# Performance work log

Hardware: AMD Instinct MI355X
Metric: run time of the kernel (lower is better)

Reference implementation:

```python
import jax, jax.numpy as jnp
import numpy as np

NEG_SLOPE = 0.2


def add_self_loops(edge_index, num_nodes):
    loop = jnp.arange(num_nodes, dtype=edge_index.dtype)
    return jnp.concatenate([edge_index, jnp.stack([loop, loop])], axis=1)


def gat_conv(x, edge_index, W, att_src, att_dst, bias, heads, out_ch, concat):
    # x: [N, F_in]; edge_index: [2, E]; W: [F_in, heads*out_ch]
    # att_src/att_dst: [heads, out_ch]; bias: [heads*out_ch] or [out_ch]
    N = x.shape[0]
    ei = add_self_loops(edge_index, N)
    src, dst = ei[0], ei[1]
    xw = (x @ W).reshape(N, heads, out_ch)          # [N, H, C]
    a_src = jnp.einsum('nhc,hc->nh', xw, att_src)    # [N, H]
    a_dst = jnp.einsum('nhc,hc->nh', xw, att_dst)    # [N, H]
    e = a_src[src] + a_dst[dst]                      # [E', H]
    e = jax.nn.leaky_relu(e, NEG_SLOPE)
    # segment softmax over edges grouped by destination node
    e_max = jax.ops.segment_max(e, dst, num_segments=N)  # [N, H]
    e_exp = jnp.exp(e - e_max[dst])
    denom = jax.ops.segment_sum(e_exp, dst, num_segments=N)  # [N, H]
    alpha = e_exp / denom[dst]                       # [E', H]
    msg = xw[src] * alpha[:, :, None]                # [E', H, C]
    out = jax.ops.segment_sum(msg, dst, num_segments=N)  # [N, H, C]
    if concat:
        out = out.reshape(N, heads * out_ch)
    else:
        out = out.mean(axis=1)
    return out + bias


def setup_inputs() -> dict:
    key = jax.random.key(0)
    ks = jax.random.split(key, 10)
    N, E = 100000, 1600000
    F_in, hid, heads, F_out = 128, 32, 4, 40
    s = 0.1
    x = jax.random.normal(ks[0], (N, F_in), dtype=jnp.float32)
    edge_index = jax.random.randint(ks[1], (2, E), 0, N, dtype=jnp.int64)
    W1 = jax.random.normal(ks[2], (F_in, heads * hid), dtype=jnp.float32) * s
    att_src1 = jax.random.normal(ks[3], (heads, hid), dtype=jnp.float32) * s
    att_dst1 = jax.random.normal(ks[4], (heads, hid), dtype=jnp.float32) * s
    b1 = jax.random.normal(ks[5], (heads * hid,), dtype=jnp.float32) * s
    W2 = jax.random.normal(ks[6], (heads * hid, F_out), dtype=jnp.float32) * s
    att_src2 = jax.random.normal(ks[7], (1, F_out), dtype=jnp.float32) * s
    att_dst2 = jax.random.normal(ks[8], (1, F_out), dtype=jnp.float32) * s
    b2 = jax.random.normal(ks[9], (F_out,), dtype=jnp.float32) * s
    return {"x": x, "edge_index": edge_index, "W1": W1, "att_src1": att_src1,
            "att_dst1": att_dst1, "b1": b1, "W2": W2, "att_src2": att_src2,
            "att_dst2": att_dst2, "b2": b2}


def reference(x, edge_index, W1, att_src1, att_dst1, b1, W2, att_src2, att_dst2, b2):
    h = gat_conv(x, edge_index, W1, att_src1, att_dst1, b1, heads=4, out_ch=32, concat=True)
    h = jax.nn.relu(h)
    out = gat_conv(h, edge_index, W2, att_src2, att_dst2, b2, heads=1, out_ch=40, concat=True)
    return out
```

## Files before the change

kernel.cpp:

```cpp
#include <hip/hip_runtime.h>
#include <hip/hip_bf16.h>

#define NEG_SLOPE 0.2f
#define LOG2E 1.4426950408889634f
#define HWREG_XCC_ID_FULL (((32 - 1) << 11) | (0 << 6) | 20)

typedef _Float16 f16;
typedef f16 f16x8 __attribute__((ext_vector_type(8)));
typedef float f32x4 __attribute__((ext_vector_type(4)));

__device__ __forceinline__ unsigned pack_h2(float a, float b) {
    union { f16 h[2]; unsigned u; } c;
    c.h[0] = (f16)a; c.h[1] = (f16)b;
    return c.u;
}

__global__ void k_init(const int* __restrict__ ei32, int npairs, int* __restrict__ flag,
                       const float* __restrict__ W1, const float* __restrict__ W2,
                       f16* __restrict__ W1t, f16* __restrict__ W2t,
                       uint4* __restrict__ deg_part4, int nzero) {
    const int b = blockIdx.x, t = threadIdx.x;
    if (b == 0) {
        __shared__ int found;
        if (t == 0) found = 0;
        __syncthreads();
        for (int i = t; i < npairs; i += 256) {
            if (ei32[2 * i + 1] != 0) found = 1;
        }
        __syncthreads();
        if (t == 0) *flag = found ? 0 : 1;
    } else if (b <= 88) {
        int o = (b - 1) * 256 + t;
        if (o < 128 * 128) {
            int n = o >> 7, k = o & 127;
            W1t[o] = (f16)W1[k * 128 + n];
        } else {
            int o2 = o - 128 * 128;
            if (o2 < 48 * 128) {
                int n = o2 >> 7, k = o2 & 127;
                W2t[o2] = (f16)(n < 40 ? W2[k * 40 + n] : 0.f);
            }
        }
    } else {
        int idx = (b - 89) * 256 + t;
        if (idx < nzero) deg_part4[idx] = (uint4){0, 0, 0, 0};
    }
}

__global__ void k_degree(const void* __restrict__ ei, const int* __restrict__ flag,
                         int* __restrict__ deg_part, unsigned* __restrict__ packed,
                         int N, int E) {
    const int base = (blockIdx.x * blockDim.x + threadIdx.x) * 4;
    if (base >= E) return;
    const int f64 = *flag;
    const int xcc = (int)(__builtin_amdgcn_s_getreg(HWREG_XCC_ID_FULL) & 7u);
    int dv[4];
    if (f64) {
        const long long* p = (const long long*)ei + E;
#pragma unroll
        for (int k = 0; k < 4; k++) dv[k] = (base + k < E) ? (int)p[base + k] : 0;
    } else {
        const int* p = (const int*)ei + E;
#pragma unroll
        for (int k = 0; k < 4; k++) dv[k] = (base + k < E) ? p[base + k] : 0;
    }
    unsigned pk[4];
#pragma unroll
    for (int k = 0; k < 4; k++) {
        int lr = (base + k < E) ? atomicAdd(&deg_part[xcc * N + dv[k]], 1) : 0;
        pk[k] = ((unsigned)dv[k] << 15) | ((unsigned)xcc << 12) | (unsigned)lr;
    }
#pragma unroll
    for (int k = 0; k < 4; k++)
        if (base + k < E) packed[base + k] = pk[k];
}

__global__ __launch_bounds__(1024) void k_scan_blk(int* __restrict__ deg_part,
                                                   int* __restrict__ offsets,
                                                   int* __restrict__ blksum, int N) {
    __shared__ int wsums[16];
    const int t = threadIdx.x;
    const int lane = t & 63;
    const int wid = t >> 6;
    int idx = blockIdx.x * 4096 + t * 4;
    int v0 = 0, v1 = 0, v2 = 0, v3 = 0;
    if (((N & 3) == 0) && (idx + 3 < N)) {
        uint4 u[8];
#pragma unroll
        for (int x = 0; x < 8; x++) u[x] = *(uint4*)&deg_part[x * N + idx];
        int p0 = 0, p1 = 0, p2 = 0, p3 = 0;
#pragma unroll
        for (int x = 0; x < 8; x++) {
            uint4 w = u[x];
            u[x] = (uint4){(unsigned)p0, (unsigned)p1, (unsigned)p2, (unsigned)p3};
            p0 += (int)w.x; p1 += (int)w.y; p2 += (int)w.z; p3 += (int)w.w;
        }
#pragma unroll
        for (int x = 0; x < 8; x++) *(uint4*)&deg_part[x * N + idx] = u[x];
        v0 = p0; v1 = p1; v2 = p2; v3 = p3;
    } else if (idx < N) {
        int vv[4] = {0, 0, 0, 0};
        for (int i = 0; i < 4; i++) {
            int d = idx + i;
            if (d >= N) break;
            int p = 0;
#pragma unroll
            for (int x = 0; x < 8; x++) {
                int t0 = deg_part[x * N + d];
                deg_part[x * N + d] = p;
                p += t0;
            }
            vv[i] = p;
        }
        v0 = vv[0]; v1 = vv[1]; v2 = vv[2]; v3 = vv[3];
    }
    int s1 = v0 + v1, s2 = s1 + v2, s3 = s2 + v3;
    int inc = s3;
#pragma unroll
    for (int off = 1; off < 64; off <<= 1) {
        int y = __shfl_up(inc, off);
        if (lane >= off) inc += y;
    }
    if (lane == 63) wsums[wid] = inc;
    __syncthreads();
    if (wid == 0) {
        int v = (lane < 16) ? wsums[lane] : 0;
        int wi = v;
#pragma unroll
        for (int off = 1; off < 16; off <<= 1) {
            int y = __shfl_up(wi, off);
            if (lane >= off) wi += y;
        }
        if (lane < 16) wsums[lane] = wi - v;
        if (lane == 15) blksum[blockIdx.x] = wi;
    }
    __syncthreads();
    int excl = wsums[wid] + (inc - s3);
    if (idx + 0 < N) offsets[idx + 1] = excl + v0;
    if (idx + 1 < N) offsets[idx + 2] = excl + s1;
    if (idx + 2 < N) offsets[idx + 3] = excl + s2;
    if (idx + 3 < N) offsets[idx + 4] = excl + s3;
}

__global__ void k_scan_top(const int* __restrict__ blksum, int* __restrict__ blkoff, int G) {
    int l = threadIdx.x;
    int v = (l < G) ? blksum[l] : 0;
    int inc = v;
#pragma unroll
    for (int off = 1; off < 64; off <<= 1) {
        int y = __shfl_up(inc, off);
        if (l >= off) inc += y;
    }
    if (l < G) blkoff[l] = inc - v;
}

__global__ void k_scan_add(int* __restrict__ offsets, const int* __restrict__ blkoff, int N) {
    int n = blockIdx.x * blockDim.x + threadIdx.x;
    if (n >= N) return;
    offsets[n + 1] += blkoff[n >> 12];
    if (n == 0) offsets[0] = 0;
}

__global__ void k_scatter(const void* __restrict__ ei, const int* __restrict__ flag,
                          const int* __restrict__ offsets, const int* __restrict__ deg_part,
                          const unsigned* __restrict__ packed, int* __restrict__ csr_src,
                          int N, int E) {
    const int base = (blockIdx.x * blockDim.x + threadIdx.x) * 4;
    if (base >= E) return;
    const int f64 = *flag;
    int sv[4];
    if (f64) {
        const long long* p = (const long long*)ei;
#pragma unroll
        for (int k = 0; k < 4; k++) sv[k] = (base + k < E) ? (int)p[base + k] : 0;
    } else {
        const int* p = (const int*)ei;
#pragma unroll
        for (int k = 0; k < 4; k++) sv[k] = (base + k < E) ? p[base + k] : 0;
    }
    unsigned pk[4];
#pragma unroll
    for (int k = 0; k < 4; k++) pk[k] = (base + k < E) ? packed[base + k] : 0;
#pragma unroll
    for (int k = 0; k < 4; k++) {
        if (base + k < E) {
            unsigned u = pk[k];
            int d = (int)(u >> 15);
            int xcc = (int)((u >> 12) & 7u);
            int lr = (int)(u & 0xFFFu);
            csr_src[offsets[d] + deg_part[xcc * N + d] + lr] = sv[k];
        }
    }
}

__global__ __launch_bounds__(256) void k_gemm1(const float* __restrict__ X,
                                               const f16* __restrict__ W1t,
                                               const float* __restrict__ as1,
                                               const float* __restrict__ ad1,
                                               f16* __restrict__ Af,
                                               float* __restrict__ aS1,
                                               float* __restrict__ aD1, int N) {
    __shared__ f16 sA[64 * 136];
    __shared__ f16 sB[128 * 136];
    const int t = threadIdx.x;
    const int row0 = blockIdx.x * 64;

    {
        int r = t >> 2, seg = t & 3;
        int row = row0 + r;
        if (row >= N) row = N - 1;
        const float4* xg = (const float4*)(X + (size_t)row * 128 + seg * 32);
        unsigned tmp[16];
#pragma unroll
        for (int j = 0; j < 8; j++) {
            float4 v = xg[j];
            tmp[2 * j]     = pack_h2(v.x, v.y);
            tmp[2 * j + 1] = pack_h2(v.z, v.w);
        }
        uint4* dst = (uint4*)&sA[r * 136 + seg * 32];
#pragma unroll
        for (int j = 0; j < 4; j++) dst[j] = ((uint4*)tmp)[j];
        int n = t >> 1, half = (t & 1) * 64;
        const uint4* src = (const uint4*)(W1t + n * 128 + half);
        uint4* dw = (uint4*)&sB[n * 136 + half];
#pragma unroll
        for (int j = 0; j < 8; j++) dw[j] = src[j];
    }
    __syncthreads();

    const int w = t >> 6, lane = t & 63, ln = lane & 15, q = lane >> 4;
    f32x4 acc[8];
#pragma unroll
    for (int c = 0; c < 8; c++) acc[c] = (f32x4){0.f, 0.f, 0.f, 0.f};

#pragma unroll
    for (int ks = 0; ks < 4; ks++) {
        f16x8 a = *(const f16x8*)&sA[(w * 16 + ln) * 136 + ks * 32 + q * 8];
#pragma unroll
        for (int c = 0; c < 8; c++) {
            f16x8 b = *(const f16x8*)&sB[(c * 16 + ln) * 136 + ks * 32 + q * 8];
            acc[c] = __builtin_amdgcn_mfma_f32_16x16x32_f16(a, b, acc[c], 0, 0, 0);
        }
    }

#pragma unroll
    for (int c = 0; c < 8; c++)
#pragma unroll
        for (int reg = 0; reg < 4; reg++) {
            int rg = row0 + w * 16 + q * 4 + reg;
            if (rg < N) Af[(size_t)rg * 128 + c * 16 + ln] = (f16)acc[c][reg];
        }

    float ps[4][4], pd[4][4];
#pragma unroll
    for (int h = 0; h < 4; h++) {
        float as_lo = as1[32 * h + ln], as_hi = as1[32 * h + 16 + ln];
        float ad_lo = ad1[32 * h + ln], ad_hi = ad1[32 * h + 16 + ln];
#pragma unroll
        for (int reg = 0; reg < 4; reg++) {
            ps[h][reg] = acc[2 * h][reg] * as_lo + acc[2 * h + 1][reg] * as_hi;
            pd[h][reg] = acc[2 * h][reg] * ad_lo + acc[2 * h + 1][reg] * ad_hi;
        }
    }
#pragma unroll
    for (int h = 0; h < 4; h++)
#pragma unroll
        for (int reg = 0; reg < 4; reg++)
#pragma unroll
            for (int off = 1; off < 16; off <<= 1) {
                ps[h][reg] += __shfl_xor(ps[h][reg], off);
                pd[h][reg] += __shfl_xor(pd[h][reg], off);
            }
#pragma unroll
    for (int h = 0; h < 4; h++) {
        if (ln == 2 * h) {
#pragma unroll
            for (int reg = 0; reg < 4; reg++) {
                int rg = row0 + w * 16 + q * 4 + reg;
                if (rg < N) aS1[rg * 4 + h] = ps[h][reg] * LOG2E;
            }
        }
        if (ln == 2 * h + 1) {
#pragma unroll
            for (int reg = 0; reg < 4; reg++) {
                int rg = row0 + w * 16 + q * 4 + reg;
                if (rg < N) aD1[rg * 4 + h] = pd[h][reg] * LOG2E;
            }
        }
    }
}

__global__ __launch_bounds__(256) void k_gemm2(const f16* __restrict__ Hf,
                                               const f16* __restrict__ W2t,
                                               const float* __restrict__ as2,
                                               const float* __restrict__ ad2,
                                               f16* __restrict__ X2f,
                                               float* __restrict__ aS2,
                                               float* __restrict__ aD2, int N) {
    __shared__ f16 sA[64 * 136];
    __shared__ f16 sB[48 * 136];
    const int t = threadIdx.x;
    const int row0 = blockIdx.x * 64;
    {
        int r = t >> 2, seg = t & 3;
        int row = row0 + r;
        if (row >= N) row = N - 1;
        const uint4* hg = (const uint4*)(Hf + (size_t)row * 128 + seg * 32);
        uint4* dst = (uint4*)&sA[r * 136 + seg * 32];
#pragma unroll
        for (int j = 0; j < 4; j++) dst[j] = hg[j];
        const uint4* wsrc = (const uint4*)W2t;
#pragma unroll
        for (int u = t; u < 768; u += 256) {
            int o = u * 8;
            int n = o >> 7, ko = o & 127;
            *(uint4*)&sB[n * 136 + ko] = wsrc[u];
        }
    }
    __syncthreads();

    const int w = t >> 6, lane = t & 63, ln = lane & 15, q = lane >> 4;
    f32x4 acc[3];
#pragma unroll
    for (int c = 0; c < 3; c++) acc[c] = (f32x4){0.f, 0.f, 0.f, 0.f};

#pragma unroll
    for (int ks = 0; ks < 4; ks++) {
        f16x8 a = *(const f16x8*)&sA[(w * 16 + ln) * 136 + ks * 32 + q * 8];
#pragma unroll
        for (int c = 0; c < 3; c++) {
            f16x8 b = *(const f16x8*)&sB[(c * 16 + ln) * 136 + ks * 32 + q * 8];
            acc[c] = __builtin_amdgcn_mfma_f32_16x16x32_f16(a, b, acc[c], 0, 0, 0);
        }
    }

#pragma unroll
    for (int c = 0; c < 3; c++) {
        int col = c * 16 + ln;
        if (col < 40) {
#pragma unroll
            for (int reg = 0; reg < 4; reg++) {
                int rg = row0 + w * 16 + q * 4 + reg;
                if (rg < N) X2f[(size_t)rg * 64 + col] = (f16)acc[c][reg];
            }
        } else {
#pragma unroll
            for (int reg = 0; reg < 4; reg++) {
                int rg = row0 + w * 16 + q * 4 + reg;
                if (rg < N) X2f[(size_t)rg * 64 + col] = (f16)0.f;
            }
        }
    }
    {
        int col = 48 + ln;
#pragma unroll
        for (int reg = 0; reg < 4; reg++) {
            int rg = row0 + w * 16 + q * 4 + reg;
            if (rg < N) X2f[(size_t)rg * 64 + col] = (f16)0.f;
        }
    }

    float ps[4], pd[4];
#pragma unroll
    for (int reg = 0; reg < 4; reg++) { ps[reg] = 0.f; pd[reg] = 0.f; }
#pragma unroll
    for (int c = 0; c < 3; c++) {
        int col = c * 16 + ln;
        float as_ = (col < 40) ? as2[col] : 0.f;
        float ad_ = (col < 40) ? ad2[col] : 0.f;
#pragma unroll
        for (int reg = 0; reg < 4; reg++) {
            ps[reg] = fmaf(acc[c][reg], as_, ps[reg]);
            pd[reg] = fmaf(acc[c][reg], ad_, pd[reg]);
        }
    }
#pragma unroll
    for (int reg = 0; reg < 4; reg++) {
#pragma unroll
        for (int off = 1; off < 16; off <<= 1) {
            ps[reg] += __shfl_xor(ps[reg], off);
            pd[reg] += __shfl_xor(pd[reg], off);
        }
        int rg = row0 + w * 16 + q * 4 + reg;
        if (rg < N) {
            if (ln == 0) aS2[rg] = ps[reg] * LOG2E;
            if (ln == 1) aD2[rg] = pd[reg] * LOG2E;
        }
    }
}

__global__ __launch_bounds__(256) void k_msg1(const int* __restrict__ offsets,
                                              const int* __restrict__ csr_src,
                                              const float* __restrict__ aS,
                                              const float* __restrict__ aD,
                                              const f16* __restrict__ Af,
                                              const float* __restrict__ b1,
                                              f16* __restrict__ Hf, int N) {
    const int lane = threadIdx.x & 63;
    const int n = blockIdx.x * 4 + (threadIdx.x >> 6);
    const bool node_ok = (n < N);
    const int g = lane >> 4;
    const int p = lane & 15;
    const int h = p >> 2;

    int b = 0, e = 0;
    float adh = 0.f;
    if (node_ok) {
        b = offsets[n];
        e = offsets[n + 1];
        adh = aD[n * 4 + h];
    }

    float acc[8];
#pragma unroll
    for (int k = 0; k < 8; k++) acc[k] = 0.f;
    float wsum = 0.f;

    if (node_ok) {
        float xs = aS[n * 4 + h] + adh;
        float ws = __builtin_amdgcn_exp2f(fmaxf(xs, NEG_SLOPE * xs));
        if (g != 0) ws = 0.f;
        const f16x8 hv = *(const f16x8*)(Af + (size_t)n * 128 + p * 8);
#pragma unroll
        for (int k = 0; k < 8; k++) acc[k] = fmaf(ws, (float)hv[k], acc[k]);
        wsum = ws;
    }

    int sreg = 0;
    if (node_ok && e > b) {
        int idx = b + lane;
        if (idx >= e) idx = e - 1;
        sreg = csr_src[idx];
    }

    int i = b;
#pragma unroll 2
    for (; i < e && (i - b) + 4 <= 64; i += 4) {
        int j = i + g;
        bool valid = (j < e);
        int s = __builtin_amdgcn_ds_bpermute((j - b) << 2, sreg);
        if (!valid) s = 0;
        float sv = aS[s * 4 + h];
        const f16x8 hv = *(const f16x8*)(Af + (size_t)s * 128 + p * 8);
        float x = sv + adh;
        float wgt = __builtin_amdgcn_exp2f(fmaxf(x, NEG_SLOPE * x));
        if (!valid) wgt = 0.f;
#pragma unroll
        for (int k = 0; k < 8; k++) acc[k] = fmaf(wgt, (float)hv[k], acc[k]);
        wsum += wgt;
    }
    for (; i < e; i += 4) {
        int j = i + g;
        bool valid = (j < e);
        int jc = valid ? j : (e - 1);
        int s = csr_src[jc];
        if (!valid) s = 0;
        float sv = aS[s * 4 + h];
        const f16x8 hv = *(const f16x8*)(Af + (size_t)s * 128 + p * 8);
        float x = sv + adh;
        float wgt = __builtin_amdgcn_exp2f(fmaxf(x, NEG_SLOPE * x));
        if (!valid) wgt = 0.f;
#pragma unroll
        for (int k = 0; k < 8; k++) acc[k] = fmaf(wgt, (float)hv[k], acc[k]);
        wsum += wgt;
    }

#pragma unroll
    for (int k = 0; k < 8; k++) {
        acc[k] += __shfl_xor(acc[k], 16);
        acc[k] += __shfl_xor(acc[k], 32);
    }
    wsum += __shfl_xor(wsum, 16);
    wsum += __shfl_xor(wsum, 32);

    if (node_ok && g == 0) {
        float inv = __builtin_amdgcn_rcpf(wsum);
        const float4* bb = (const float4*)(b1 + p * 8);
        float4 b0 = bb[0], b4 = bb[1];
        float bv[8] = {b0.x, b0.y, b0.z, b0.w, b4.x, b4.y, b4.z, b4.w};
        union { f16 h8[8]; uint4 u; } o;
#pragma unroll
        for (int k = 0; k < 8; k++) {
            float v = fmaf(acc[k], inv, bv[k]);
            o.h8[k] = (f16)fmaxf(v, 0.f);
        }
        *(uint4*)(Hf + (size_t)n * 128 + p * 8) = o.u;
    }
}

__global__ __launch_bounds__(256) void k_msg2(const int* __restrict__ offsets,
                                              const int* __restrict__ csr_src,
                                              const float* __restrict__ aS,
                                              const float* __restrict__ aD,
                                              const f16* __restrict__ X2f,
                                              const float* __restrict__ b2,
                                              float* __restrict__ OUT, int N) {
    const int lane = threadIdx.x & 63;
    const int n = blockIdx.x * 4 + (threadIdx.x >> 6);
    const bool node_ok = (n < N);
    const int g = lane >> 3;
    const int p = lane & 7;

    int b = 0, e = 0;
    float adh = 0.f;
    if (node_ok) {
        b = offsets[n];
        e = offsets[n + 1];
        adh = aD[n];
    }

    float acc[8];
#pragma unroll
    for (int k = 0; k < 8; k++) acc[k] = 0.f;
    float wsum = 0.f;

    if (node_ok) {
        float xs = aS[n] + adh;
        float ws = __builtin_amdgcn_exp2f(fmaxf(xs, NEG_SLOPE * xs));
        if (g != 0) ws = 0.f;
        const f16x8 hv = *(const f16x8*)(X2f + (size_t)n * 64 + p * 8);
#pragma unroll
        for (int k = 0; k < 8; k++) acc[k] = fmaf(ws, (float)hv[k], acc[k]);
        wsum = ws;
    }

    int sreg = 0;
    if (node_ok && e > b) {
        int idx = b + lane;
        if (idx >= e) idx = e - 1;
        sreg = csr_src[idx];
    }

    int i = b;
#pragma unroll 2
    for (; i < e && (i - b) + 8 <= 64; i += 8) {
        int j = i + g;
        bool valid = (j < e);
        int s = __builtin_amdgcn_ds_bpermute((j - b) << 2, sreg);
        if (!valid) s = 0;
        float sv = aS[s];
        const f16x8 hv = *(const f16x8*)(X2f + (size_t)s * 64 + p * 8);
        float x = sv + adh;
        float wgt = __builtin_amdgcn_exp2f(fmaxf(x, NEG_SLOPE * x));
        if (!valid) wgt = 0.f;
#pragma unroll
        for (int k = 0; k < 8; k++) acc[k] = fmaf(wgt, (float)hv[k], acc[k]);
        wsum += wgt;
    }
    for (; i < e; i += 8) {
        int j = i + g;
        bool valid = (j < e);
        int jc = valid ? j : (e - 1);
        int s = csr_src[jc];
        if (!valid) s = 0;
        float sv = aS[s];
        const f16x8 hv = *(const f16x8*)(X2f + (size_t)s * 64 + p * 8);
        float x = sv + adh;
        float wgt = __builtin_amdgcn_exp2f(fmaxf(x, NEG_SLOPE * x));
        if (!valid) wgt = 0.f;
#pragma unroll
        for (int k = 0; k < 8; k++) acc[k] = fmaf(wgt, (float)hv[k], acc[k]);
        wsum += wgt;
    }

#pragma unroll
    for (int k = 0; k < 8; k++) {
        acc[k] += __shfl_xor(acc[k], 8);
        acc[k] += __shfl_xor(acc[k], 16);
        acc[k] += __shfl_xor(acc[k], 32);
    }
    wsum += __shfl_xor(wsum, 8);
    wsum += __shfl_xor(wsum, 16);
    wsum += __shfl_xor(wsum, 32);

    if (node_ok && g == 0 && p < 5) {
        float inv = __builtin_amdgcn_rcpf(wsum);
        const float4* bb = (const float4*)(b2 + p * 8);
        float4 b0 = bb[0], b4 = bb[1];
        float bv[8] = {b0.x, b0.y, b0.z, b0.w, b4.x, b4.y, b4.z, b4.w};
        float4 o0, o1;
        o0.x = fmaf(acc[0], inv, bv[0]); o0.y = fmaf(acc[1], inv, bv[1]);
        o0.z = fmaf(acc[2], inv, bv[2]); o0.w = fmaf(acc[3], inv, bv[3]);
        o1.x = fmaf(acc[4], inv, bv[4]); o1.y = fmaf(acc[5], inv, bv[5]);
        o1.z = fmaf(acc[6], inv, bv[6]); o1.w = fmaf(acc[7], inv, bv[7]);
        float* op = OUT + (size_t)n * 40 + p * 8;
        *(float4*)op = o0;
        *(float4*)(op + 4) = o1;
    }
}

extern "C" void kernel_launch(void* const* d_in, const int* in_sizes, int n_in,
                              void* d_out, int out_size, void* d_ws, size_t ws_size,
                              hipStream_t stream) {
    const float* x   = (const float*)d_in[0];
    const void*  ei  = d_in[1];
    const float* W1  = (const float*)d_in[2];
    const float* as1 = (const float*)d_in[3];
    const float* ad1 = (const float*)d_in[4];
    const float* b1  = (const float*)d_in[5];
    const float* W2  = (const float*)d_in[6];
    const float* as2 = (const float*)d_in[7];
    const float* ad2 = (const float*)d_in[8];
    const float* b2  = (const float*)d_in[9];
    float* out = (float*)d_out;

    const int N = in_sizes[0] / 128;
    const int E = in_sizes[1] / 2;

    char* w = (char*)d_ws;
    auto alloc = [&](size_t bytes) {
        char* p = w;
        w += (bytes + 15) & ~(size_t)15;
        return p;
    };
    int* flag        = (int*)alloc(16);
    int* offsets     = (int*)alloc((size_t)(N + 1) * 4);
    int* deg_part    = (int*)alloc((size_t)N * 8 * 4);
    unsigned* packed = (unsigned*)alloc((size_t)E * 4);
    int* csr_src     = (int*)alloc((size_t)E * 4);
    int* blksum      = (int*)alloc(64 * 4);
    int* blkoff      = (int*)alloc(64 * 4);
    float* aS1       = (float*)alloc((size_t)N * 4 * 4);
    float* aD1       = (float*)alloc((size_t)N * 4 * 4);
    float* aS2       = (float*)alloc((size_t)N * 4);
    float* aD2       = (float*)alloc((size_t)N * 4);
    f16* W1t         = (f16*)alloc(128 * 128 * 2);
    f16* W2t         = (f16*)alloc(48 * 128 * 2);
    f16* Af          = (f16*)alloc((size_t)N * 128 * 2);
    f16* X2f         = (f16*)alloc((size_t)N * 64 * 2);
    f16* Hf          = (f16*)alloc((size_t)N * 128 * 2);

    const int nzero = 2 * N;
    k_init<<<89 + (nzero + 255) / 256, 256, 0, stream>>>(
        (const int*)ei, 1024, flag, W1, W2, W1t, W2t, (uint4*)deg_part, nzero);

    k_degree<<<(E + 1023) / 1024, 256, 0, stream>>>(ei, flag, deg_part, packed, N, E);
    const int G = (N + 4095) / 4096;
    k_scan_blk<<<G, 1024, 0, stream>>>(deg_part, offsets, blksum, N);
    k_scan_top<<<1, 64, 0, stream>>>(blksum, blkoff, G);
    k_scan_add<<<(N + 255) / 256, 256, 0, stream>>>(offsets, blkoff, N);
    k_scatter<<<(E + 1023) / 1024, 256, 0, stream>>>(ei, flag, offsets, deg_part,
                                                     packed, csr_src, N, E);

    const int gb = (N + 63) / 64;
    k_gemm1<<<gb, 256, 0, stream>>>(x, W1t, as1, ad1, Af, aS1, aD1, N);
    k_msg1<<<(N + 3) / 4, 256, 0, stream>>>(offsets, csr_src, aS1, aD1, Af, b1, Hf, N);

    k_gemm2<<<gb, 256, 0, stream>>>(Hf, W2t, as2, ad2, X2f, aS2, aD2, N);
    k_msg2<<<(N + 3) / 4, 256, 0, stream>>>(offsets, csr_src, aS2, aD2, X2f, b2, out, N);
}
```

Baseline: 395.2 us.

## Fuse CSR construction kernels into one cooperative grid-synced kernel

Result: slower. 977.6 us (+147.4%).

```diff
diff --git a/kernel.cpp b/kernel.cpp
--- a/kernel.cpp
+++ b/kernel.cpp
@@ -1,9 +1,14 @@
 #include <hip/hip_runtime.h>
 #include <hip/hip_bf16.h>
+#include <hip/hip_cooperative_groups.h>
+
+namespace cg = cooperative_groups;
 
 #define NEG_SLOPE 0.2f
 #define LOG2E 1.4426950408889634f
 #define HWREG_XCC_ID_FULL (((32 - 1) << 11) | (0 << 6) | 20)
+
+#define CSR_GRID 1024
 
 typedef _Float16 f16;
 typedef f16 f16x8 __attribute__((ext_vector_type(8)));
@@ -15,74 +20,77 @@
     return c.u;
 }
 
-__global__ void k_init(const int* __restrict__ ei32, int npairs, int* __restrict__ flag,
-                       const float* __restrict__ W1, const float* __restrict__ W2,
-                       f16* __restrict__ W1t, f16* __restrict__ W2t,
-                       uint4* __restrict__ deg_part4, int nzero) {
-    const int b = blockIdx.x, t = threadIdx.x;
-    if (b == 0) {
-        __shared__ int found;
+__global__ __launch_bounds__(256) void k_csr(const int* __restrict__ ei32,
+                                             const void* __restrict__ ei,
+                                             int* __restrict__ flag,
+                                             const float* __restrict__ W1,
+                                             const float* __restrict__ W2,
+                                             f16* __restrict__ W1t,
+                                             f16* __restrict__ W2t,
+                                             int* __restrict__ deg_part,
+                                             unsigned* __restrict__ packed,
+                                             int* __restrict__ offsets,
+                                             int* __restrict__ blksum,
+                                             int* __restrict__ blkoff,
+                                             int* __restrict__ csr_src,
+                                             int N, int E) {
+    cg::grid_group grid = cg::this_grid();
+    __shared__ int wsums[4];
+    __shared__ int found;
+    const int B = blockIdx.x, t = threadIdx.x;
+    const int gsize = gridDim.x * blockDim.x;
+    const int gid = B * blockDim.x + t;
+    const int lane = t & 63, wid = t >> 6;
+
+    if (B == 0) {
         if (t == 0) found = 0;
         __syncthreads();
-        for (int i = t; i < npairs; i += 256) {
+        for (int i = t; i < 1024; i += 256)
             if (ei32[2 * i + 1] != 0) found = 1;
-        }
         __syncthreads();
         if (t == 0) *flag = found ? 0 : 1;
-    } else if (b <= 88) {
-        int o = (b - 1) * 256 + t;
+    }
+    for (int o = gid; o < 128 * 128 + 48 * 128; o += gsize) {
         if (o < 128 * 128) {
             int n = o >> 7, k = o & 127;
             W1t[o] = (f16)W1[k * 128 + n];
         } else {
             int o2 = o - 128 * 128;
-            if (o2 < 48 * 128) {
-                int n = o2 >> 7, k = o2 & 127;
-                W2t[o2] = (f16)(n < 40 ? W2[k * 40 + n] : 0.f);
-            }
-        }
-    } else {
-        int idx = (b - 89) * 256 + t;
-        if (idx < nzero) deg_part4[idx] = (uint4){0, 0, 0, 0};
-    }
-}
-
-__global__ void k_degree(const void* __restrict__ ei, const int* __restrict__ flag,
-                         int* __restrict__ deg_part, unsigned* __restrict__ packed,
-                         int N, int E) {
-    const int base = (blockIdx.x * blockDim.x + threadIdx.x) * 4;
-    if (base >= E) return;
+            int n = o2 >> 7, k = o2 & 127;
+            W2t[o2] = (f16)(n < 40 ? W2[k * 40 + n] : 0.f);
+        }
+    }
+    {
+        uint4* dp4 = (uint4*)deg_part;
+        for (int i = gid; i < 2 * N; i += gsize) dp4[i] = (uint4){0, 0, 0, 0};
+    }
+    grid.sync();
+
     const int f64 = *flag;
     const int xcc = (int)(__builtin_amdgcn_s_getreg(HWREG_XCC_ID_FULL) & 7u);
-    int dv[4];
-    if (f64) {
-        const long long* p = (const long long*)ei + E;
-#pragma unroll
-        for (int k = 0; k < 4; k++) dv[k] = (base + k < E) ? (int)p[base + k] : 0;
-    } else {
-        const int* p = (const int*)ei + E;
-#pragma unroll
-        for (int k = 0; k < 4; k++) dv[k] = (base + k < E) ? p[base + k] : 0;
-    }
-    unsigned pk[4];
-#pragma unroll
-    for (int k = 0; k < 4; k++) {
-        int lr = (base + k < E) ? atomicAdd(&deg_part[xcc * N + dv[k]], 1) : 0;
-        pk[k] = ((unsigned)dv[k] << 15) | ((unsigned)xcc << 12) | (unsigned)lr;
-    }
-#pragma unroll
-    for (int k = 0; k < 4; k++)
-        if (base + k < E) packed[base + k] = pk[k];
-}
-
-__global__ __launch_bounds__(1024) void k_scan_blk(int* __restrict__ deg_part,
-                                                   int* __restrict__ offsets,
-                                                   int* __restrict__ blksum, int N) {
-    __shared__ int wsums[16];
-    const int t = threadIdx.x;
-    const int lane = t & 63;
-    const int wid = t >> 6;
-    int idx = blockIdx.x * 4096 + t * 4;
+    for (int base = gid * 4; base < E; base += gsize * 4) {
+        int dv[4];
+        if (f64) {
+            const long long* p = (const long long*)ei + E;
+#pragma unroll
+            for (int k = 0; k < 4; k++) dv[k] = (base + k < E) ? (int)p[base + k] : 0;
+        } else {
+            const int* p = (const int*)ei + E;
+#pragma unroll
+            for (int k = 0; k < 4; k++) dv[k] = (base + k < E) ? p[base + k] : 0;
+        }
+#pragma unroll
+        for (int k = 0; k < 4; k++) {
+            if (base + k < E) {
+                int lr = atomicAdd(&deg_part[xcc * N + dv[k]], 1);
+                packed[base + k] = ((unsigned)dv[k] << 15) | ((unsigned)xcc << 12) |
+                                   (unsigned)lr;
+            }
+        }
+    }
+    grid.sync();
+
+    const int idx = gid * 4;
     int v0 = 0, v1 = 0, v2 = 0, v3 = 0;
     if (((N & 3) == 0) && (idx + 3 < N)) {
         uint4 u[8];
@@ -114,7 +122,7 @@
         }
         v0 = vv[0]; v1 = vv[1]; v2 = vv[2]; v3 = vv[3];
     }
-    int s1 = v0 + v1, s2 = s1 + v2, s3 = s2 + v3;
+    const int s1 = v0 + v1, s2 = s1 + v2, s3 = s2 + v3;
     int inc = s3;
 #pragma unroll
     for (int off = 1; off < 64; off <<= 1) {
@@ -124,71 +132,81 @@
     if (lane == 63) wsums[wid] = inc;
     __syncthreads();
     if (wid == 0) {
-        int v = (lane < 16) ? wsums[lane] : 0;
+        int v = (lane < 4) ? wsums[lane] : 0;
         int wi = v;
 #pragma unroll
-        for (int off = 1; off < 16; off <<= 1) {
+        for (int off = 1; off < 4; off <<= 1) {
             int y = __shfl_up(wi, off);
             if (lane >= off) wi += y;
         }
-        if (lane < 16) wsums[lane] = wi - v;
-        if (lane == 15) blksum[blockIdx.x] = wi;
+        if (lane < 4) wsums[lane] = wi - v;
+        if (lane == 3) blksum[B] = wi;
     }
     __syncthreads();
-    int excl = wsums[wid] + (inc - s3);
-    if (idx + 0 < N) offsets[idx + 1] = excl + v0;
-    if (idx + 1 < N) offsets[idx + 2] = excl + s1;
-    if (idx + 2 < N) offsets[idx + 3] = excl + s2;
-    if (idx + 3 < N) offsets[idx + 4] = excl + s3;
-}
-
-__global__ void k_scan_top(const int* __restrict__ blksum, int* __restrict__ blkoff, int G) {
-    int l = threadIdx.x;
-    int v = (l < G) ? blksum[l] : 0;
-    int inc = v;
-#pragma unroll
-    for (int off = 1; off < 64; off <<= 1) {
-        int y = __shfl_up(inc, off);
-        if (l >= off) inc += y;
-    }
-    if (l < G) blkoff[l] = inc - v;
-}
-
-__global__ void k_scan_add(int* __restrict__ offsets, const int* __restrict__ blkoff, int N) {
-    int n = blockIdx.x * blockDim.x + threadIdx.x;
-    if (n >= N) return;
-    offsets[n + 1] += blkoff[n >> 12];
-    if (n == 0) offsets[0] = 0;
-}
-
-__global__ void k_scatter(const void* __restrict__ ei, const int* __restrict__ flag,
-                          const int* __restrict__ offsets, const int* __restrict__ deg_part,
-                          const unsigned* __restrict__ packed, int* __restrict__ csr_src,
-                          int N, int E) {
-    const int base = (blockIdx.x * blockDim.x + threadIdx.x) * 4;
-    if (base >= E) return;
-    const int f64 = *flag;
-    int sv[4];
-    if (f64) {
-        const long long* p = (const long long*)ei;
-#pragma unroll
-        for (int k = 0; k < 4; k++) sv[k] = (base + k < E) ? (int)p[base + k] : 0;
-    } else {
-        const int* p = (const int*)ei;
-#pragma unroll
-        for (int k = 0; k < 4; k++) sv[k] = (base + k < E) ? p[base + k] : 0;
-    }
-    unsigned pk[4];
-#pragma unroll
-    for (int k = 0; k < 4; k++) pk[k] = (base + k < E) ? packed[base + k] : 0;
-#pragma unroll
-    for (int k = 0; k < 4; k++) {
-        if (base + k < E) {
-            unsigned u = pk[k];
-            int d = (int)(u >> 15);
-            int xcc = (int)((u >> 12) & 7u);
-            int lr = (int)(u & 0xFFFu);
-            csr_src[offsets[d] + deg_part[xcc * N + d] + lr] = sv[k];
+    const int excl_local = wsums[wid] + (inc - s3);
+    grid.sync();
+
+    if (B == 0) {
+        int i = t * 4;
+        int b0 = blksum[i], b1 = blksum[i + 1], b2 = blksum[i + 2], b3 = blksum[i + 3];
+        int t1 = b0 + b1, t2 = t1 + b2, t3 = t2 + b3;
+        int inc2 = t3;
+#pragma unroll
+        for (int off = 1; off < 64; off <<= 1) {
+            int y = __shfl_up(inc2, off);
+            if (lane >= off) inc2 += y;
+        }
+        if (lane == 63) wsums[wid] = inc2;
+        __syncthreads();
+        if (wid == 0) {
+            int v = (lane < 4) ? wsums[lane] : 0;
+            int wi = v;
+#pragma unroll
+            for (int off = 1; off < 4; off <<= 1) {
+                int y = __shfl_up(wi, off);
+                if (lane >= off) wi += y;
+            }
+            if (lane < 4) wsums[lane] = wi - v;
+        }
+        __syncthreads();
+        int ex2 = wsums[wid] + (inc2 - t3);
+        blkoff[i] = ex2;
+        blkoff[i + 1] = ex2 + b0;
+        blkoff[i + 2] = ex2 + t1;
+        blkoff[i + 3] = ex2 + t2;
+    }
+    grid.sync();
+
+    {
+        const int boff = blkoff[B] + excl_local;
+        if (idx + 0 < N) offsets[idx + 1] = boff + v0;
+        if (idx + 1 < N) offsets[idx + 2] = boff + s1;
+        if (idx + 2 < N) offsets[idx + 3] = boff + s2;
+        if (idx + 3 < N) offsets[idx + 4] = boff + s3;
+        if (gid == 0) offsets[0] = 0;
+    }
+    grid.sync();
+
+    for (int base = gid * 4; base < E; base += gsize * 4) {
+        int sv[4];
+        if (f64) {
+            const long long* p = (const long long*)ei;
+#pragma unroll
+            for (int k = 0; k < 4; k++) sv[k] = (base + k < E) ? (int)p[base + k] : 0;
+        } else {
+            const int* p = (const int*)ei;
+#pragma unroll
+            for (int k = 0; k < 4; k++) sv[k] = (base + k < E) ? p[base + k] : 0;
+        }
+#pragma unroll
+        for (int k = 0; k < 4; k++) {
+            if (base + k < E) {
+                unsigned u = packed[base + k];
+                int d = (int)(u >> 15);
+                int xc = (int)((u >> 12) & 7u);
+                int lr = (int)(u & 0xFFFu);
+                csr_src[offsets[d] + deg_part[xc * N + d] + lr] = sv[k];
+            }
         }
     }
 }
@@ -618,8 +636,8 @@
     int* deg_part    = (int*)alloc((size_t)N * 8 * 4);
     unsigned* packed = (unsigned*)alloc((size_t)E * 4);
     int* csr_src     = (int*)alloc((size_t)E * 4);
-    int* blksum      = (int*)alloc(64 * 4);
-    int* blkoff      = (int*)alloc(64 * 4);
+    int* blksum      = (int*)alloc((size_t)CSR_GRID * 4);
+    int* blkoff      = (int*)alloc((size_t)CSR_GRID * 4);
     float* aS1       = (float*)alloc((size_t)N * 4 * 4);
     float* aD1       = (float*)alloc((size_t)N * 4 * 4);
     float* aS2       = (float*)alloc((size_t)N * 4);
@@ -630,17 +648,18 @@
     f16* X2f         = (f16*)alloc((size_t)N * 64 * 2);
     f16* Hf          = (f16*)alloc((size_t)N * 128 * 2);
 
-    const int nzero = 2 * N;
-    k_init<<<89 + (nzero + 255) / 256, 256, 0, stream>>>(
-        (const int*)ei, 1024, flag, W1, W2, W1t, W2t, (uint4*)deg_part, nzero);
-
-    k_degree<<<(E + 1023) / 1024, 256, 0, stream>>>(ei, flag, deg_part, packed, N, E);
-    const int G = (N + 4095) / 4096;
-    k_scan_blk<<<G, 1024, 0, stream>>>(deg_part, offsets, blksum, N);
-    k_scan_top<<<1, 64, 0, stream>>>(blksum, blkoff, G);
-    k_scan_add<<<(N + 255) / 256, 256, 0, stream>>>(offsets, blkoff, N);
-    k_scatter<<<(E + 1023) / 1024, 256, 0, stream>>>(ei, flag, offsets, deg_part,
-                                                     packed, csr_src, N, E);
+    {
+        const int* ei32 = (const int*)ei;
+        const void* eiv = ei;
+        int Nv = N, Ev = E;
+        void* args[] = {(void*)&ei32, (void*)&eiv, (void*)&flag,
+                        (void*)&W1, (void*)&W2, (void*)&W1t, (void*)&W2t,
+                        (void*)&deg_part, (void*)&packed, (void*)&offsets,
+                        (void*)&blksum, (void*)&blkoff, (void*)&csr_src,
+                        (void*)&Nv, (void*)&Ev};
+        hipLaunchCooperativeKernel((void*)k_csr, dim3(CSR_GRID), dim3(256),
+                                   args, 0, stream);
+    }
 
     const int gb = (N + 63) / 64;
     k_gemm1<<<gb, 256, 0, stream>>>(x, W1t, as1, ad1, Af, aS1, aD1, N);
```

## Fuse three-kernel prefix scan into single-pass decoupled scan

Applied to the files above, without the earlier changes.

Result: no change. 393.7 us (-0.4%).

```diff
diff --git a/kernel.cpp b/kernel.cpp
--- a/kernel.cpp
+++ b/kernel.cpp
@@ -18,11 +18,13 @@
 __global__ void k_init(const int* __restrict__ ei32, int npairs, int* __restrict__ flag,
                        const float* __restrict__ W1, const float* __restrict__ W2,
                        f16* __restrict__ W1t, f16* __restrict__ W2t,
-                       uint4* __restrict__ deg_part4, int nzero) {
+                       uint4* __restrict__ deg_part4, int nzero,
+                       int* __restrict__ partials) {
     const int b = blockIdx.x, t = threadIdx.x;
     if (b == 0) {
         __shared__ int found;
         if (t == 0) found = 0;
+        if (t < 64) partials[t] = 0;
         __syncthreads();
         for (int i = t; i < npairs; i += 256) {
             if (ei32[2 * i + 1] != 0) found = 1;
@@ -75,14 +77,16 @@
         if (base + k < E) packed[base + k] = pk[k];
 }
 
-__global__ __launch_bounds__(1024) void k_scan_blk(int* __restrict__ deg_part,
-                                                   int* __restrict__ offsets,
-                                                   int* __restrict__ blksum, int N) {
+__global__ __launch_bounds__(1024) void k_scan(int* __restrict__ deg_part,
+                                               int* __restrict__ offsets,
+                                               int* __restrict__ partials, int N) {
     __shared__ int wsums[16];
+    __shared__ int bprefix;
     const int t = threadIdx.x;
     const int lane = t & 63;
     const int wid = t >> 6;
-    int idx = blockIdx.x * 4096 + t * 4;
+    const int B = blockIdx.x;
+    int idx = B * 4096 + t * 4;
     int v0 = 0, v1 = 0, v2 = 0, v3 = 0;
     if (((N & 3) == 0) && (idx + 3 < N)) {
         uint4 u[8];
@@ -114,7 +118,7 @@
         }
         v0 = vv[0]; v1 = vv[1]; v2 = vv[2]; v3 = vv[3];
     }
-    int s1 = v0 + v1, s2 = s1 + v2, s3 = s2 + v3;
+    const int s1 = v0 + v1, s2 = s1 + v2, s3 = s2 + v3;
     int inc = s3;
 #pragma unroll
     for (int off = 1; off < 64; off <<= 1) {
@@ -132,33 +136,30 @@
             if (lane >= off) wi += y;
         }
         if (lane < 16) wsums[lane] = wi - v;
-        if (lane == 15) blksum[blockIdx.x] = wi;
+        int tot = __shfl(wi, 15);
+        if (lane == 0)
+            __hip_atomic_store(&partials[B], tot + 1, __ATOMIC_RELEASE,
+                               __HIP_MEMORY_SCOPE_AGENT);
+        int pre = 0;
+        for (int i = lane; i < B; i += 64) {
+            int vr;
+            do {
+                vr = __hip_atomic_load(&partials[i], __ATOMIC_ACQUIRE,
+                                       __HIP_MEMORY_SCOPE_AGENT);
+            } while (vr == 0);
+            pre += vr - 1;
+        }
+#pragma unroll
+        for (int off = 1; off < 64; off <<= 1) pre += __shfl_xor(pre, off);
+        if (lane == 0) bprefix = pre;
     }
     __syncthreads();
-    int excl = wsums[wid] + (inc - s3);
+    const int excl = bprefix + wsums[wid] + (inc - s3);
     if (idx + 0 < N) offsets[idx + 1] = excl + v0;
     if (idx + 1 < N) offsets[idx + 2] = excl + s1;
     if (idx + 2 < N) offsets[idx + 3] = excl + s2;
     if (idx + 3 < N) offsets[idx + 4] = excl + s3;
-}
-
-__global__ void k_scan_top(const int* __restrict__ blksum, int* __restrict__ blkoff, int G) {
-    int l = threadIdx.x;
-    int v = (l < G) ? blksum[l] : 0;
-    int inc = v;
-#pragma unroll
-    for (int off = 1; off < 64; off <<= 1) {
-        int y = __shfl_up(inc, off);
-        if (l >= off) inc += y;
-    }
-    if (l < G) blkoff[l] = inc - v;
-}
-
-__global__ void k_scan_add(int* __restrict__ offsets, const int* __restrict__ blkoff, int N) {
-    int n = blockIdx.x * blockDim.x + threadIdx.x;
-    if (n >= N) return;
-    offsets[n + 1] += blkoff[n >> 12];
-    if (n == 0) offsets[0] = 0;
+    if (B == 0 && t == 0) offsets[0] = 0;
 }
 
 __global__ void k_scatter(const void* __restrict__ ei, const int* __restrict__ flag,
@@ -618,8 +619,7 @@
     int* deg_part    = (int*)alloc((size_t)N * 8 * 4);
     unsigned* packed = (unsigned*)alloc((size_t)E * 4);
     int* csr_src     = (int*)alloc((size_t)E * 4);
-    int* blksum      = (int*)alloc(64 * 4);
-    int* blkoff      = (int*)alloc(64 * 4);
+    int* partials    = (int*)alloc(64 * 4);
     float* aS1       = (float*)alloc((size_t)N * 4 * 4);
     float* aD1       = (float*)alloc((size_t)N * 4 * 4);
     float* aS2       = (float*)alloc((size_t)N * 4);
@@ -632,13 +632,11 @@
 
     const int nzero = 2 * N;
     k_init<<<89 + (nzero + 255) / 256, 256, 0, stream>>>(
-        (const int*)ei, 1024, flag, W1, W2, W1t, W2t, (uint4*)deg_part, nzero);
+        (const int*)ei, 1024, flag, W1, W2, W1t, W2t, (uint4*)deg_part, nzero, partials);
 
     k_degree<<<(E + 1023) / 1024, 256, 0, stream>>>(ei, flag, deg_part, packed, N, E);
     const int G = (N + 4095) / 4096;
-    k_scan_blk<<<G, 1024, 0, stream>>>(deg_part, offsets, blksum, N);
-    k_scan_top<<<1, 64, 0, stream>>>(blksum, blkoff, G);
-    k_scan_add<<<(N + 255) / 256, 256, 0, stream>>>(offsets, blkoff, N);
+    k_scan<<<G, 1024, 0, stream>>>(deg_part, offsets, partials, N);
     k_scatter<<<(E + 1023) / 1024, 256, 0, stream>>>(ei, flag, offsets, deg_part,
                                                      packed, csr_src, N, E);
 
```
